# Performance work log

Measured on AMD Instinct MI355X. Metric: run time of the kernel, lower is better.

The kernel has to match this reference:

```python
import jax, jax.numpy as jnp
import numpy as np

BC, N, F, D = 16, 2048, 128, 128
N_EDGES = 65536
NEG_INF = -1e16
LEAK = 0.1


def setup_inputs() -> dict:
    key = jax.random.key(0)
    k_h, k_w, k_r, k_c = jax.random.split(key, 4)
    h = jax.random.normal(k_h, (BC, N, F), dtype=jnp.float32)
    # xavier_normal with gain 1.414
    w_std = 1.414 * np.sqrt(2.0 / (F + D))
    W = jax.random.normal(k_w, (F, D), dtype=jnp.float32) * w_std
    row = jax.random.randint(k_r, (N_EDGES,), 0, N, dtype=jnp.int64)
    col = jax.random.randint(k_c, (N_EDGES,), 0, N, dtype=jnp.int64)
    return {"h": h, "W": W, "row": row, "col": col}


def reference(h, W, row, col):
    bc, n, f = h.shape
    # z = h @ W : [bc, N, D]
    z = jnp.einsum("bnf,fd->bnd", h, W)
    # dense inner-product attention scores [bc, N, N]
    att = jnp.einsum("bnd,bmd->bnm", z, z)
    # leaky_relu(0.1)
    att = jnp.where(att > 0, att, LEAK * att)
    # sparse adjacency mask built from COO indices
    mask = jnp.zeros((n, n), dtype=att.dtype).at[row, col].set(1.0)
    att = att * mask[None, :, :]
    # masked_fill where value == 0 (non-edges, and incidental exact zeros)
    att = jnp.where(att == 0.0, NEG_INF, att)
    att = jax.nn.softmax(att, axis=2)
    # aggregate: [bc, N, N] @ [bc, N, D]
    return jnp.einsum("bnm,bmd->bnd", att, z)
```

## Files before the change

### kernel.cpp

```cpp
#include <hip/hip_runtime.h>

#define BC 16
#define NN 2048
#define FF 128
#define DD 128
#define NEDGES 65536
#define NEG_INF -1e16f
#define LEAK 0.1f
#define CAPR 128

__global__ void __launch_bounds__(256) zgemm_kernel(const float* __restrict__ h,
                                                    const float* __restrict__ W,
                                                    float* __restrict__ z,
                                                    unsigned int* __restrict__ mask,
                                                    int* __restrict__ deg) {
    const int tid = threadIdx.x;
    const int gid = blockIdx.x * 256 + tid;
    if (gid < NN * NN / 32) mask[gid] = 0u;
    if (gid < NN) deg[gid] = 0;

    __shared__ float hs[32][FF];
    const size_t row0 = (size_t)blockIdx.x * 32;
    const float4* hv = (const float4*)(h + row0 * FF);
    float4* hsv = (float4*)&hs[0][0];
#pragma unroll
    for (int i = 0; i < 4; ++i) hsv[tid + 256 * i] = hv[tid + 256 * i];
    __syncthreads();

    const int c0 = (tid & 31) * 4;
    const int r0 = (tid >> 5) * 4;
    float acc[4][4] = {};
    for (int f = 0; f < FF; f += 4) {
        float4 a[4], bb[4];
#pragma unroll
        for (int r = 0; r < 4; ++r) a[r] = *(const float4*)&hs[r0 + r][f];
#pragma unroll
        for (int k = 0; k < 4; ++k) bb[k] = *(const float4*)&W[(f + k) * DD + c0];
#pragma unroll
        for (int r = 0; r < 4; ++r) {
            acc[r][0] += a[r].x * bb[0].x + a[r].y * bb[1].x + a[r].z * bb[2].x + a[r].w * bb[3].x;
            acc[r][1] += a[r].x * bb[0].y + a[r].y * bb[1].y + a[r].z * bb[2].y + a[r].w * bb[3].y;
            acc[r][2] += a[r].x * bb[0].z + a[r].y * bb[1].z + a[r].z * bb[2].z + a[r].w * bb[3].z;
            acc[r][3] += a[r].x * bb[0].w + a[r].y * bb[1].w + a[r].z * bb[2].w + a[r].w * bb[3].w;
        }
    }
#pragma unroll
    for (int r = 0; r < 4; ++r)
        *(float4*)&z[(row0 + r0 + r) * DD + c0] =
            make_float4(acc[r][0], acc[r][1], acc[r][2], acc[r][3]);
}

__global__ void edge_kernel(const int* __restrict__ row, const int* __restrict__ col,
                            unsigned int* __restrict__ mask,
                            unsigned short* __restrict__ hits_g,
                            int* __restrict__ deg) {
    const int e = blockIdx.x * blockDim.x + threadIdx.x;
    if (e < NEDGES) {
        const int r = row[e], c = col[e];
        const unsigned int key = (unsigned int)r * NN + (unsigned int)c;
        const unsigned int bit = 1u << (key & 31u);
        const unsigned int old = atomicOr(&mask[key >> 5], bit);
        if (!(old & bit)) {
            const int slot = atomicAdd(&deg[r], 1);
            if (slot < CAPR) hits_g[r * CAPR + slot] = (unsigned short)c;
        }
    }
}

__global__ void __launch_bounds__(256) gat_kernel(const float* __restrict__ z,
                                                  const unsigned short* __restrict__ hits_g,
                                                  const int* __restrict__ deg,
                                                  float* __restrict__ out) {
    const int tid = threadIdx.x, wv = tid >> 6, ln = tid & 63;
    const int blk = blockIdx.x;
    const int b = ((blk & 7) << 1) | (wv & 1);
    const int n = ((blk >> 3) << 1) | (wv >> 1);
    const int eq = ln >> 3, hq = ln & 7;

    const float* zb = z + ((size_t)b << 18);
    const int nh = min(deg[n], CAPR);
    const unsigned short* hrow = hits_g + n * CAPR;

    const float4* znp = (const float4*)(zb + ((size_t)n << 7) + (hq << 4));
    const float4 a0 = znp[0], a1 = znp[1], a2 = znp[2], a3 = znp[3];

    float m = NEG_INF, l = 0.f;
    float4 acc0 = make_float4(0.f, 0.f, 0.f, 0.f), acc1 = acc0, acc2 = acc0, acc3 = acc0;

#pragma unroll 2
    for (int c0 = 0; c0 < nh; c0 += 8) {
        const int e = c0 + eq;
        const int he = hrow[min(e, nh - 1)];
        const float4* zc = (const float4*)(zb + ((size_t)he << 7) + (hq << 4));
        const float4 v0 = zc[0], v1 = zc[1], v2 = zc[2], v3 = zc[3];
        float pt = a0.x * v0.x + a0.y * v0.y + a0.z * v0.z + a0.w * v0.w
                 + a1.x * v1.x + a1.y * v1.y + a1.z * v1.z + a1.w * v1.w
                 + a2.x * v2.x + a2.y * v2.y + a2.z * v2.z + a2.w * v2.w
                 + a3.x * v3.x + a3.y * v3.y + a3.z * v3.z + a3.w * v3.w;
        pt += __shfl_xor(pt, 1, 64);
        pt += __shfl_xor(pt, 2, 64);
        pt += __shfl_xor(pt, 4, 64);
        float sv = pt > 0.f ? pt : LEAK * pt;
        if (sv == 0.f || e >= nh) sv = NEG_INF;

        const float mnew = fmaxf(m, sv);
        const float alpha = __expf(m - mnew);
        const float pr = __expf(sv - mnew);
        l = l * alpha + pr;
        acc0.x = acc0.x * alpha + pr * v0.x; acc0.y = acc0.y * alpha + pr * v0.y;
        acc0.z = acc0.z * alpha + pr * v0.z; acc0.w = acc0.w * alpha + pr * v0.w;
        acc1.x = acc1.x * alpha + pr * v1.x; acc1.y = acc1.y * alpha + pr * v1.y;
        acc1.z = acc1.z * alpha + pr * v1.z; acc1.w = acc1.w * alpha + pr * v1.w;
        acc2.x = acc2.x * alpha + pr * v2.x; acc2.y = acc2.y * alpha + pr * v2.y;
        acc2.z = acc2.z * alpha + pr * v2.z; acc2.w = acc2.w * alpha + pr * v2.w;
        acc3.x = acc3.x * alpha + pr * v3.x; acc3.y = acc3.y * alpha + pr * v3.y;
        acc3.z = acc3.z * alpha + pr * v3.z; acc3.w = acc3.w * alpha + pr * v3.w;
        m = mnew;
    }

    float M = m;
#pragma unroll
    for (int off = 8; off <= 32; off <<= 1) M = fmaxf(M, __shfl_xor(M, off, 64));

    if (nh > 0 && M > 0.5f * NEG_INF) {
        const float al = __expf(m - M);
        l *= al;
        acc0.x *= al; acc0.y *= al; acc0.z *= al; acc0.w *= al;
        acc1.x *= al; acc1.y *= al; acc1.z *= al; acc1.w *= al;
        acc2.x *= al; acc2.y *= al; acc2.z *= al; acc2.w *= al;
        acc3.x *= al; acc3.y *= al; acc3.z *= al; acc3.w *= al;
#pragma unroll
        for (int off = 8; off <= 32; off <<= 1) {
            l += __shfl_xor(l, off, 64);
            acc0.x += __shfl_xor(acc0.x, off, 64); acc0.y += __shfl_xor(acc0.y, off, 64);
            acc0.z += __shfl_xor(acc0.z, off, 64); acc0.w += __shfl_xor(acc0.w, off, 64);
            acc1.x += __shfl_xor(acc1.x, off, 64); acc1.y += __shfl_xor(acc1.y, off, 64);
            acc1.z += __shfl_xor(acc1.z, off, 64); acc1.w += __shfl_xor(acc1.w, off, 64);
            acc2.x += __shfl_xor(acc2.x, off, 64); acc2.y += __shfl_xor(acc2.y, off, 64);
            acc2.z += __shfl_xor(acc2.z, off, 64); acc2.w += __shfl_xor(acc2.w, off, 64);
            acc3.x += __shfl_xor(acc3.x, off, 64); acc3.y += __shfl_xor(acc3.y, off, 64);
            acc3.z += __shfl_xor(acc3.z, off, 64); acc3.w += __shfl_xor(acc3.w, off, 64);
        }
        const float inv = 1.f / l;
        acc0.x *= inv; acc0.y *= inv; acc0.z *= inv; acc0.w *= inv;
        acc1.x *= inv; acc1.y *= inv; acc1.z *= inv; acc1.w *= inv;
        acc2.x *= inv; acc2.y *= inv; acc2.z *= inv; acc2.w *= inv;
        acc3.x *= inv; acc3.y *= inv; acc3.z *= inv; acc3.w *= inv;
    } else {
        acc0 = make_float4(0.f, 0.f, 0.f, 0.f); acc1 = acc0; acc2 = acc0; acc3 = acc0;
        for (int mm = 0; mm < NN; ++mm) {
            const float4* zr = (const float4*)(zb + ((size_t)mm << 7) + (hq << 4));
            const float4 t0 = zr[0], t1 = zr[1], t2 = zr[2], t3 = zr[3];
            acc0.x += t0.x; acc0.y += t0.y; acc0.z += t0.z; acc0.w += t0.w;
            acc1.x += t1.x; acc1.y += t1.y; acc1.z += t1.z; acc1.w += t1.w;
            acc2.x += t2.x; acc2.y += t2.y; acc2.z += t2.z; acc2.w += t2.w;
            acc3.x += t3.x; acc3.y += t3.y; acc3.z += t3.z; acc3.w += t3.w;
        }
        const float s = 1.f / NN;
        acc0.x *= s; acc0.y *= s; acc0.z *= s; acc0.w *= s;
        acc1.x *= s; acc1.y *= s; acc1.z *= s; acc1.w *= s;
        acc2.x *= s; acc2.y *= s; acc2.z *= s; acc2.w *= s;
        acc3.x *= s; acc3.y *= s; acc3.z *= s; acc3.w *= s;
    }

    if (eq < 4) {
        float4 o = acc0;
        if (eq == 1) o = acc1;
        if (eq == 2) o = acc2;
        if (eq == 3) o = acc3;
        *(float4*)(out + (((size_t)b * NN + n) << 7) + (hq << 4) + (eq << 2)) = o;
    }
}

extern "C" void kernel_launch(void* const* d_in, const int* in_sizes, int n_in,
                              void* d_out, int out_size, void* d_ws, size_t ws_size,
                              hipStream_t stream) {
    const float* h = (const float*)d_in[0];
    const float* W = (const float*)d_in[1];
    const int* row = (const int*)d_in[2];
    const int* col = (const int*)d_in[3];
    float* out = (float*)d_out;

    char* ws = (char*)d_ws;
    float* z = (float*)ws;
    unsigned int* mask = (unsigned int*)(ws + (size_t)16 * 1024 * 1024);
    unsigned short* hits_g = (unsigned short*)(ws + (size_t)16 * 1024 * 1024 + 512 * 1024);
    int* deg = (int*)(ws + (size_t)17 * 1024 * 1024);

    zgemm_kernel<<<(BC * NN) / 32, 256, 0, stream>>>(h, W, z, mask, deg);
    edge_kernel<<<NEDGES / 256, 256, 0, stream>>>(row, col, mask, hits_g, deg);
    gat_kernel<<<(BC * NN) / 4, 256, 0, stream>>>(z, hits_g, deg, out);
}
```

Baseline: 159.6 us.

## Fold edge scatter into z GEMM launch and build sorted CSR from bitmask

Edge bit-setting atomics now run in 256 extra blocks of the z GEMM kernel, and the mask is cleared with a memset. A new per-row kernel builds the neighbor lists by popcount plus a wave prefix scan over the adjacency bitmask, replacing the per-edge atomicAdd on degree counters. Neighbor lists become column-sorted and deterministic, which may slightly improve gather locality in the attention kernel. The cost is an added memset and a second small kernel that reads the full 512KB bitmask.

```diff
diff --git a/kernel.cpp b/kernel.cpp
--- a/kernel.cpp
+++ b/kernel.cpp
@@ -9,18 +9,24 @@
 #define LEAK 0.1f
 #define CAPR 128
 
-__global__ void __launch_bounds__(256) zgemm_kernel(const float* __restrict__ h,
+__global__ void __launch_bounds__(256) zedge_kernel(const float* __restrict__ h,
                                                     const float* __restrict__ W,
                                                     float* __restrict__ z,
-                                                    unsigned int* __restrict__ mask,
-                                                    int* __restrict__ deg) {
+                                                    const int* __restrict__ row,
+                                                    const int* __restrict__ col,
+                                                    unsigned int* __restrict__ mask) {
     const int tid = threadIdx.x;
-    const int gid = blockIdx.x * 256 + tid;
-    if (gid < NN * NN / 32) mask[gid] = 0u;
-    if (gid < NN) deg[gid] = 0;
+    const int blk = blockIdx.x;
+
+    if (blk < 256) {
+        const int e = blk * 256 + tid;
+        const unsigned int key = (unsigned int)row[e] * NN + (unsigned int)col[e];
+        atomicOr(&mask[key >> 5], 1u << (key & 31u));
+        return;
+    }
 
     __shared__ float hs[32][FF];
-    const size_t row0 = (size_t)blockIdx.x * 32;
+    const size_t row0 = (size_t)(blk - 256) * 32;
     const float4* hv = (const float4*)(h + row0 * FF);
     float4* hsv = (float4*)&hs[0][0];
 #pragma unroll
@@ -50,20 +56,26 @@
             make_float4(acc[r][0], acc[r][1], acc[r][2], acc[r][3]);
 }
 
-__global__ void edge_kernel(const int* __restrict__ row, const int* __restrict__ col,
-                            unsigned int* __restrict__ mask,
-                            unsigned short* __restrict__ hits_g,
-                            int* __restrict__ deg) {
-    const int e = blockIdx.x * blockDim.x + threadIdx.x;
-    if (e < NEDGES) {
-        const int r = row[e], c = col[e];
-        const unsigned int key = (unsigned int)r * NN + (unsigned int)c;
-        const unsigned int bit = 1u << (key & 31u);
-        const unsigned int old = atomicOr(&mask[key >> 5], bit);
-        if (!(old & bit)) {
-            const int slot = atomicAdd(&deg[r], 1);
-            if (slot < CAPR) hits_g[r * CAPR + slot] = (unsigned short)c;
-        }
+__global__ void __launch_bounds__(256) csr_kernel(const unsigned int* __restrict__ mask,
+                                                  unsigned short* __restrict__ hits_g,
+                                                  int* __restrict__ deg) {
+    const int tid = threadIdx.x, wv = tid >> 6, ln = tid & 63;
+    const int n = blockIdx.x * 4 + wv;
+    unsigned int bits = mask[n * 64 + ln];
+    const int cnt = __popc(bits);
+    int pre = cnt;
+#pragma unroll
+    for (int off = 1; off <= 32; off <<= 1) {
+        const int t = __shfl_up(pre, off, 64);
+        if (ln >= off) pre += t;
+    }
+    if (ln == 63) deg[n] = pre;
+    int slot = pre - cnt;
+    while (bits) {
+        const int bit = __ffs(bits) - 1;
+        bits &= bits - 1;
+        if (slot < CAPR) hits_g[n * CAPR + slot] = (unsigned short)(ln * 32 + bit);
+        ++slot;
     }
 }
 
@@ -187,7 +199,8 @@
     unsigned short* hits_g = (unsigned short*)(ws + (size_t)16 * 1024 * 1024 + 512 * 1024);
     int* deg = (int*)(ws + (size_t)17 * 1024 * 1024);
 
-    zgemm_kernel<<<(BC * NN) / 32, 256, 0, stream>>>(h, W, z, mask, deg);
-    edge_kernel<<<NEDGES / 256, 256, 0, stream>>>(row, col, mask, hits_g, deg);
+    hipMemsetAsync(mask, 0, (size_t)NN * NN / 8, stream);
+    zedge_kernel<<<1280, 256, 0, stream>>>(h, W, z, row, col, mask);
+    csr_kernel<<<NN / 4, 256, 0, stream>>>(mask, hits_g, deg);
     gat_kernel<<<(BC * NN) / 4, 256, 0, stream>>>(z, hits_g, deg, out);
 }
```

Measured after the change: 150.4 us, median of 2. -5.8%, faster.
